# Performance work log

Hardware: AMD Instinct MI355X
Metric: run time of the kernel (lower is better)

Reference implementation:

```python
import jax, jax.numpy as jnp
import numpy as np

D, H, HD, F, A, P, NB, MD = 1024, 16, 64, 2816, 64, 30, 32, 128
B, L = 4, 1024


def _rel_bucket(rel, num_buckets=NB, max_distance=MD):
    # T5 relative position bucket, bidirectional=False (decoder self-attn)
    rel = -jnp.minimum(rel, 0)
    max_exact = num_buckets // 2
    is_small = rel < max_exact
    large = max_exact + (
        jnp.log(jnp.maximum(rel, 1).astype(jnp.float32) / max_exact)
        / np.log(max_distance / max_exact)
        * (num_buckets - max_exact)
    ).astype(jnp.int32)
    large = jnp.minimum(large, num_buckets - 1)
    return jnp.where(is_small, rel, large)


def _rmsnorm(x, scale, eps=1e-6):
    var = jnp.mean(jnp.square(x), axis=-1, keepdims=True)
    return x * jax.lax.rsqrt(var + eps) * scale


def _attn(x, kv, wq, wk, wv, wo, mask, bias, pk, pv):
    # x: [B,Lq,D], kv: [B,Lk,D], prefix pk/pv: [B,P,H,HD]
    hd = wq.shape[-1]
    q = jnp.einsum('bqd,dhe->bqhe', x, wq) * (hd ** -0.5)
    k = jnp.einsum('bkd,dhe->bkhe', kv, wk)
    v = jnp.einsum('bkd,dhe->bkhe', kv, wv)
    k = jnp.concatenate([pk, k], axis=1)  # prefix KV prepended
    v = jnp.concatenate([pv, v], axis=1)
    logits = jnp.einsum('bqhe,bkhe->bhqk', q, k).astype(jnp.float32)
    p = pk.shape[1]
    if bias is not None:
        logits = logits + jnp.pad(bias, ((0, 0), (0, 0), (0, 0), (p, 0)))
    mask = jnp.pad(mask, ((0, 0), (0, 0), (0, 0), (p, 0)), constant_values=True)
    logits = jnp.where(mask, logits, jnp.float32(-1e10))
    w = jax.nn.softmax(logits, axis=-1).astype(x.dtype)
    o = jnp.einsum('bhqk,bkhe->bqhe', w, v)
    return jnp.einsum('bqhe,hed->bqd', o, wo)


def setup_inputs() -> dict:
    key = jax.random.key(0)
    ks = jax.random.split(key, 24)
    s = D ** -0.5
    inp = {
        'inputs': jax.random.normal(ks[0], (B, L, D), jnp.float32),
        'encoded': jax.random.normal(ks[1], (B, L, D), jnp.float32),
        'adapter_wd': jax.random.normal(ks[2], (B, D, A), jnp.float32) * s,
        'adapter_wu': jax.random.normal(ks[3], (B, A, D), jnp.float32) * (A ** -0.5),
        'adapter_bd': jax.random.normal(ks[4], (B, A), jnp.float32) * 0.02,
        'adapter_bu': jax.random.normal(ks[5], (B, D), jnp.float32) * 0.02,
        'prefix_key': jax.random.normal(ks[6], (B, 2, P, H, HD), jnp.float32),
        'prefix_value': jax.random.normal(ks[7], (B, 2, P, H, HD), jnp.float32),
        'ln1': jnp.ones((D,), jnp.float32),
        'ln2': jnp.ones((D,), jnp.float32),
        'ln3': jnp.ones((D,), jnp.float32),
        'sa_wq': jax.random.normal(ks[8], (D, H, HD), jnp.float32) * s,
        'sa_wk': jax.random.normal(ks[9], (D, H, HD), jnp.float32) * s,
        'sa_wv': jax.random.normal(ks[10], (D, H, HD), jnp.float32) * s,
        'sa_wo': jax.random.normal(ks[11], (H, HD, D), jnp.float32) * s,
        'ca_wq': jax.random.normal(ks[12], (D, H, HD), jnp.float32) * s,
        'ca_wk': jax.random.normal(ks[13], (D, H, HD), jnp.float32) * s,
        'ca_wv': jax.random.normal(ks[14], (D, H, HD), jnp.float32) * s,
        'ca_wo': jax.random.normal(ks[15], (H, HD, D), jnp.float32) * s,
        'relpos': jax.random.normal(ks[16], (H, NB), jnp.float32) * 0.1,
        'mlp_wi0': jax.random.normal(ks[17], (D, F), jnp.float32) * s,
        'mlp_wi1': jax.random.normal(ks[18], (D, F), jnp.float32) * s,
        'mlp_wo': jax.random.normal(ks[19], (F, D), jnp.float32) * (F ** -0.5),
        'decoder_mask': jnp.broadcast_to(jnp.tril(jnp.ones((L, L), bool))[None, None], (B, 1, L, L)),
        'encoder_decoder_mask': jnp.ones((B, 1, L, L), bool),
    }
    return inp


def reference(inputs, encoded, adapter_wd, adapter_wu, adapter_bd, adapter_bu,
              prefix_key, prefix_value, ln1, ln2, ln3,
              sa_wq, sa_wk, sa_wv, sa_wo, ca_wq, ca_wk, ca_wv, ca_wo,
              relpos, mlp_wi0, mlp_wi1, mlp_wo,
              decoder_mask, encoder_decoder_mask):
    l = inputs.shape[1]
    pos = jnp.arange(l)
    buckets = _rel_bucket(pos[None, :] - pos[:, None])  # [L,L]
    bias = relpos[:, buckets][None]                      # [1,H,L,L]
    # self-attention with prefix + relative bias
    x = _rmsnorm(inputs, ln1)
    x = _attn(x, x, sa_wq, sa_wk, sa_wv, sa_wo, decoder_mask, bias,
              prefix_key[:, 0], prefix_value[:, 0])
    x = x + inputs
    # cross-attention with prefix
    y = _rmsnorm(x, ln2)
    y = _attn(y, encoded, ca_wq, ca_wk, ca_wv, ca_wo, encoder_decoder_mask, None,
              prefix_key[:, 1], prefix_value[:, 1])
    y = y + x
    # gated-gelu MLP + per-example adapter
    lz = _rmsnorm(y, ln3)
    z = (jax.nn.gelu(lz @ mlp_wi0) * (lz @ mlp_wi1)) @ mlp_wo
    az = jnp.einsum('bld,bda->bla', lz, adapter_wd) + adapter_bd[:, None]
    az = jax.nn.gelu(az)
    az = jnp.einsum('bla,bad->bld', az, adapter_wu) + adapter_bu[:, None]
    z = z + az
    return z + y
```

## Files before the change

### kernel.cpp

```cpp
#include <hip/hip_runtime.h>

typedef unsigned short u16;
typedef __attribute__((ext_vector_type(8))) __bf16 bf16x8;
typedef __attribute__((ext_vector_type(4))) float f32x4;

__device__ __forceinline__ float bf2f(u16 u) {
  union { unsigned int i; float f; } v; v.i = ((unsigned int)u) << 16; return v.f;
}
__device__ __forceinline__ u16 f2bf(float f) {
  unsigned int x = __float_as_uint(f);
  unsigned int r = (x + 0x7fffu + ((x >> 16) & 1u)) >> 16;
  return (u16)r;
}
__device__ __forceinline__ u16 f2bf_fast(float f) {
  return (u16)((__float_as_uint(f) + 0x8000u) >> 16);
}
__device__ __forceinline__ float gelu_f(float x) {
  float u = 0.7978845608028654f * (x + 0.044715f * x * x * x);
  float t = 1.0f - 2.0f / (__expf(2.0f * u) + 1.0f);
  return 0.5f * x * (1.0f + t);
}
__device__ __forceinline__ void gl_lds16(const u16* g, u16* l) {
  __builtin_amdgcn_global_load_lds(
      (const __attribute__((address_space(1))) unsigned int*)g,
      (__attribute__((address_space(3))) unsigned int*)l, 16, 0, 0);
}

__global__ __launch_bounds__(256) void cast_bf16_k(const float* __restrict__ in,
                                                   u16* __restrict__ out, int n4) {
  int i = blockIdx.x * 256 + threadIdx.x;
  if (i >= n4) return;
  float4 v = ((const float4*)in)[i];
  ushort4 o;
  o.x = f2bf(v.x); o.y = f2bf(v.y); o.z = f2bf(v.z); o.w = f2bf(v.w);
  ((ushort4*)out)[i] = o;
}

__global__ __launch_bounds__(256) void transpose_k(
    const float* __restrict__ in, u16* __restrict__ out, int R, int C,
    long isb, long osb) {
  __shared__ u16 tile[32][33];
  in += (size_t)blockIdx.z * isb;
  out += (size_t)blockIdx.z * osb;
  int c0 = blockIdx.x * 32, r0 = blockIdx.y * 32;
  int tx = threadIdx.x & 31, ty = threadIdx.x >> 5;
#pragma unroll
  for (int i = 0; i < 4; ++i) {
    int rr = r0 + ty + i * 8;
    if (rr < R && c0 + tx < C) tile[ty + i * 8][tx] = f2bf(in[(size_t)rr * C + c0 + tx]);
  }
  __syncthreads();
#pragma unroll
  for (int i = 0; i < 4; ++i) {
    int cc = c0 + ty + i * 8;
    if (cc < C && r0 + tx < R) out[(size_t)cc * R + r0 + tx] = tile[tx][ty + i * 8];
  }
}

__global__ __launch_bounds__(256) void bias_tab_k(const float* __restrict__ relpos,
                                                  float* __restrict__ tab) {
  int idx = blockIdx.x * 256 + threadIdx.x;
  int h = idx >> 10, d = idx & 1023;
  int bucket;
  if (d < 16) bucket = d;
  else {
    int lb = 16 + (int)(logf((float)d * (1.0f / 16.0f)) * (16.0f / logf(8.0f)));
    bucket = lb < 31 ? lb : 31;
  }
  tab[idx] = relpos[h * 32 + bucket];
}

__global__ __launch_bounds__(256) void prefix_fill_k(
    const float* __restrict__ pK, const float* __restrict__ pV,
    u16* __restrict__ Kd, u16* __restrict__ Vtd, int sSel) {
  int idx = blockIdx.x * 256 + threadIdx.x;
  int e = idx & 63, p = (idx >> 6) & 31, h = (idx >> 11) & 15, b = idx >> 15;
  int key = (p < 30) ? p : (1024 + p);
  float kv = 0.f, vv = 0.f;
  if (p < 30) {
    size_t src = ((((size_t)(b * 2 + sSel)) * 30 + p) * 16 + h) * 64 + e;
    kv = pK[src]; vv = pV[src];
  }
  Kd[(((size_t)(b * 16 + h)) * 1056 + key) * 64 + e] = f2bf(kv);
  Vtd[(((size_t)(b * 16 + h)) * 64 + e) * 1056 + key] = f2bf(vv);
}

__global__ __launch_bounds__(256) void rmsnorm_k(const float* __restrict__ in,
                                                 const float* __restrict__ scale,
                                                 u16* __restrict__ out) {
  const int D = 1024;
  size_t base = (size_t)blockIdx.x * D;
  int t = threadIdx.x;
  float x[4];
#pragma unroll
  for (int i = 0; i < 4; ++i) x[i] = in[base + t + i * 256];
  float s = x[0] * x[0] + x[1] * x[1] + x[2] * x[2] + x[3] * x[3];
#pragma unroll
  for (int off = 1; off < 64; off <<= 1) s += __shfl_xor(s, off, 64);
  __shared__ float ws4[4];
  if ((t & 63) == 0) ws4[t >> 6] = s;
  __syncthreads();
  float tot = ws4[0] + ws4[1] + ws4[2] + ws4[3];
  float r = rsqrtf(tot * (1.0f / D) + 1e-6f);
#pragma unroll
  for (int i = 0; i < 4; ++i) {
    int c = t + i * 256;
    out[base + c] = f2bf(x[i] * r * scale[c]);
  }
}

__global__ __launch_bounds__(256) void gelumul_k(const u16* __restrict__ g2,
                                                 u16* __restrict__ g) {
  int i = blockIdx.x * 256 + threadIdx.x;
  int m = i / 352, f8 = i - m * 352;
  size_t b0 = (size_t)m * 5632 + f8 * 8;
  uint4 h0 = *(const uint4*)(g2 + b0);
  uint4 h1 = *(const uint4*)(g2 + b0 + 2816);
  const u16* p0 = (const u16*)&h0;
  const u16* p1 = (const u16*)&h1;
  uint4 ov;
  u16* po = (u16*)&ov;
#pragma unroll
  for (int j = 0; j < 8; ++j) po[j] = f2bf(gelu_f(bf2f(p0[j])) * bf2f(p1[j]));
  *(uint4*)(g + (size_t)m * 2816 + f8 * 8) = ov;
}

template <int MODE>
__global__ __launch_bounds__(256) void gemm97(
    const u16* __restrict__ A, const u16* __restrict__ Bt, void* __restrict__ out,
    void* __restrict__ out2, void* __restrict__ out3,
    const float* __restrict__ res1, int M, int N, int K, float alpha) {
  const int BK = 32;
  __shared__ __align__(16) u16 As[128 * 32];
  __shared__ __align__(16) u16 Bs[128 * 32];

  const int t = threadIdx.x;
  const int wave = t >> 6, lane = t & 63;
  const int m0 = blockIdx.y * 128, n0 = blockIdx.x * 128;
  const int fr = lane & 15, fq = lane >> 4;
  const int wm = (wave >> 1) * 64, wn = (wave & 1) * 64;

  const int srow = wave * 32 + (lane >> 2);
  const int scol = (lane & 3) * 8;
  const u16* ag0 = A + (size_t)(m0 + srow) * K + scol;
  const u16* ag1 = ag0 + (size_t)16 * K;
  const u16* bg0 = Bt + (size_t)(n0 + srow) * K + scol;
  const u16* bg1 = bg0 + (size_t)16 * K;
  u16* al0 = &As[(wave * 32) * 32];
  u16* al1 = &As[(wave * 32 + 16) * 32];
  u16* bl0 = &Bs[(wave * 32) * 32];
  u16* bl1 = &Bs[(wave * 32 + 16) * 32];

  f32x4 acc[16];
#pragma unroll
  for (int i = 0; i < 16; ++i) acc[i] = (f32x4){0.f, 0.f, 0.f, 0.f};

  for (int k0 = 0; k0 < K; k0 += BK) {
    gl_lds16(ag0 + k0, al0);
    gl_lds16(ag1 + k0, al1);
    gl_lds16(bg0 + k0, bl0);
    gl_lds16(bg1 + k0, bl1);
    __syncthreads();
    bf16x8 af[4], bf[4];
#pragma unroll
    for (int i = 0; i < 4; ++i)
      af[i] = *(const bf16x8*)&As[(wm + i * 16 + fr) * 32 + fq * 8];
#pragma unroll
    for (int j = 0; j < 4; ++j)
      bf[j] = *(const bf16x8*)&Bs[(wn + j * 16 + fr) * 32 + fq * 8];
#pragma unroll
    for (int i = 0; i < 4; ++i)
#pragma unroll
      for (int j = 0; j < 4; ++j)
        acc[i * 4 + j] = __builtin_amdgcn_mfma_f32_16x16x32_bf16(
            af[i], bf[j], acc[i * 4 + j], 0, 0, 0);
    __syncthreads();
  }

#pragma unroll
  for (int i = 0; i < 4; ++i) {
#pragma unroll
    for (int rr = 0; rr < 4; ++rr) {
      long gm = (long)m0 + wm + i * 16 + fq * 4 + rr;
#pragma unroll
      for (int j = 0; j < 4; ++j) {
        int gn = n0 + wn + j * 16 + fr;
        float v = acc[i * 4 + j][rr];
        size_t oi = (size_t)gm * N + gn;
        if (MODE == 0) ((float*)out)[oi] = v;
        if (MODE == 2) ((u16*)out)[oi] = f2bf(v);
        if (MODE == 3) ((float*)out)[oi] = v + res1[oi];
        if (MODE == 8) {
          int b = (int)(gm >> 10), l = (int)(gm & 1023), h = gn >> 6, e = gn & 63;
          ((u16*)out)[(((size_t)(b * 16 + h)) * 1024 + l) * 64 + e] = f2bf(v * alpha);
        }
        if (MODE == 11) {
          int b = (int)(gm >> 10), l = (int)(gm & 1023);
          int sec = gn >> 10, nn = gn & 1023, h = nn >> 6, e = nn & 63;
          if (sec == 0)
            ((u16*)out)[(((size_t)(b * 16 + h)) * 1024 + l) * 64 + e] = f2bf(v * alpha);
          else if (sec == 1)
            ((u16*)out2)[(((size_t)(b * 16 + h)) * 1056 + 30 + l) * 64 + e] = f2bf(v);
          else
            ((u16*)out3)[(((size_t)(b * 16 + h)) * 64 + e) * 1056 + 30 + l] = f2bf(v);
        }
        if (MODE == 12) {
          int b = (int)(gm >> 10), l = (int)(gm & 1023);
          int sec = gn >> 10, nn = gn & 1023, h = nn >> 6, e = nn & 63;
          if (sec == 0)
            ((u16*)out)[(((size_t)(b * 16 + h)) * 1056 + 30 + l) * 64 + e] = f2bf(v);
          else
            ((u16*)out2)[(((size_t)(b * 16 + h)) * 64 + e) * 1056 + 30 + l] = f2bf(v);
        }
      }
    }
  }
}

template <int MODE>
__global__ __launch_bounds__(256) void gemm_bt(
    const u16* __restrict__ A, const u16* __restrict__ Bt, void* __restrict__ out,
    const float* __restrict__ res1, const float* __restrict__ res2,
    const float* __restrict__ bias, int M, int N, int K,
    long Asb, long Bsb, long bsb, long r1sb, long r2sb, long osb) {
  const int BM = 128, BK = 32, LP = 40;
  __shared__ __align__(16) u16 As[BM * LP];
  __shared__ __align__(16) u16 Bs[BM * LP];

  const int t = threadIdx.x;
  const int m0 = blockIdx.y * BM;
  const int n0 = blockIdx.x * 128;
  const int bz = blockIdx.z;
  A += (size_t)bz * Asb;
  Bt += (size_t)bz * Bsb;

  f32x4 acc[16];
#pragma unroll
  for (int i = 0; i < 16; ++i) acc[i] = (f32x4){0.f, 0.f, 0.f, 0.f};
  const int wave = t >> 6, lane = t & 63;
  const int wm = (wave >> 1) * 64, wn = (wave & 1) * 64;
  const int fr = lane & 15, fq = lane >> 4;

  for (int k0 = 0; k0 < K; k0 += BK) {
#pragma unroll
    for (int i = 0; i < 2; ++i) {
      int idx = (i * 256 + t) * 8;
      int row = idx >> 5, col = idx & 31;
      *(uint4*)&As[row * LP + col] =
          *(const uint4*)(A + (size_t)(m0 + row) * K + k0 + col);
      uint4 bv = {0u, 0u, 0u, 0u};
      if (n0 + row < N) bv = *(const uint4*)(Bt + (size_t)(n0 + row) * K + k0 + col);
      *(uint4*)&Bs[row * LP + col] = bv;
    }
    __syncthreads();
    bf16x8 af[4], bfr[4];
#pragma unroll
    for (int i = 0; i < 4; ++i)
      af[i] = *(const bf16x8*)&As[(wm + i * 16 + fr) * LP + fq * 8];
#pragma unroll
    for (int j = 0; j < 4; ++j)
      bfr[j] = *(const bf16x8*)&Bs[(wn + j * 16 + fr) * LP + fq * 8];
#pragma unroll
    for (int i = 0; i < 4; ++i)
#pragma unroll
      for (int j = 0; j < 4; ++j)
        acc[i * 4 + j] = __builtin_amdgcn_mfma_f32_16x16x32_bf16(
            af[i], bfr[j], acc[i * 4 + j], 0, 0, 0);
    __syncthreads();
  }

#pragma unroll
  for (int i = 0; i < 4; ++i) {
#pragma unroll
    for (int rr = 0; rr < 4; ++rr) {
      long gm = (long)m0 + wm + i * 16 + fq * 4 + rr;
#pragma unroll
      for (int j = 0; j < 4; ++j) {
        int gn = n0 + wn + j * 16 + fr;
        if (gn >= N) continue;
        float v = acc[i * 4 + j][rr];
        size_t oi = (size_t)bz * osb + (size_t)gm * N + gn;
        size_t ri = (size_t)gm * N + gn;
        if (MODE == 6) ((u16*)out)[oi] = f2bf(gelu_f(v + bias[(size_t)bz * bsb + gn]));
        if (MODE == 7)
          ((float*)out)[oi] = v + bias[(size_t)bz * bsb + gn] +
                              res1[(size_t)bz * r1sb + ri] +
                              res2[(size_t)bz * r2sb + ri];
      }
    }
  }
}

template <bool IS_SELF>
__global__ __launch_bounds__(256) void fattn_k(
    const u16* __restrict__ Qg, const u16* __restrict__ Kg,
    const u16* __restrict__ Vtg, const float* __restrict__ bias_tab,
    u16* __restrict__ Out) {
  const int L = 1024, P = 30, KC = 1056;
  const int flat = blockIdx.x;
  const int wg = (flat & 7) * 64 + (flat >> 3);
  const int q0b = (wg & 7) * 128;
  const int h = (wg >> 3) & 15, b = wg >> 7;
  const int t = threadIdx.x, wave = t >> 6, lane = t & 63;
  const int fr = lane & 15, fq = lane >> 4;
  const int q0w = q0b + wave * 32;

  __shared__ float bTs[IS_SELF ? 1024 : 4];
  __shared__ __align__(16) u16 Ps[4][32][40];

  if (IS_SELF) {
#pragma unroll
    for (int i = 0; i < 4; ++i) bTs[t + i * 256] = bias_tab[h * 1024 + t + i * 256];
    __syncthreads();
  }

  const u16* qptr = Qg + (((size_t)(b * 16 + h)) * L + q0w + fr) * 64 + fq * 8;
  bf16x8 qa0 = *(const bf16x8*)qptr;
  bf16x8 qa1 = *(const bf16x8*)(qptr + 32);
  bf16x8 qb0 = *(const bf16x8*)(qptr + 16 * 64);
  bf16x8 qb1 = *(const bf16x8*)(qptr + 16 * 64 + 32);

  f32x4 oA[4], oB[4];
#pragma unroll
  for (int i = 0; i < 4; ++i) {
    oA[i] = (f32x4){0.f, 0.f, 0.f, 0.f};
    oB[i] = (f32x4){0.f, 0.f, 0.f, 0.f};
  }
  f32x4 olA = (f32x4){0.f, 0.f, 0.f, 0.f};
  f32x4 olB = (f32x4){0.f, 0.f, 0.f, 0.f};
  bf16x8 ones;
  {
    u16 one = 0x3F80;
#pragma unroll
    for (int i = 0; i < 8; ++i) ((u16*)&ones)[i] = one;
  }

  const int nk = IS_SELF ? (P + q0b + 128) : (P + L);
  const int nch = (nk + 31) >> 5;
  const u16* kp = Kg + ((size_t)(b * 16 + h)) * KC * 64 + (size_t)fr * 64 + fq * 8;
  const u16* vp = Vtg + ((size_t)(b * 16 + h)) * 64 * KC + (size_t)fr * KC + fq * 8;

  bf16x8 kf0 = *(const bf16x8*)(kp + 0);
  bf16x8 kf1 = *(const bf16x8*)(kp + 32);
  bf16x8 kf2 = *(const bf16x8*)(kp + 16 * 64);
  bf16x8 kf3 = *(const bf16x8*)(kp + 16 * 64 + 32);

  auto smax = [&](f32x4* s, int k0, int qoff, int rb) {
    const bool full = IS_SELF ? (k0 >= 32 && k0 + 31 - P <= qoff)
                              : (k0 + 31 < P + L);
    if (full) {
      if (IS_SELF) {
#pragma unroll
        for (int reg = 0; reg < 4; ++reg) {
          const int qq = qoff + fq * 4 + reg;
          s[0][reg] += bTs[qq - (k0 + fr - P)];
          s[1][reg] += bTs[qq - (k0 + 16 + fr - P)];
        }
      }
    } else {
#pragma unroll
      for (int reg = 0; reg < 4; ++reg) {
        const int qq = qoff + fq * 4 + reg;
#pragma unroll
        for (int t2 = 0; t2 < 2; ++t2) {
          const int kvi = k0 + t2 * 16 + fr;
          float sv = s[t2][reg];
          if (IS_SELF) {
            const int lk = kvi - P;
            if (lk >= 0) {
              if (lk <= qq) sv += bTs[qq - lk];
              else sv = -3.0e38f;
            }
          } else {
            if (kvi >= P + L) sv = -3.0e38f;
          }
          s[t2][reg] = sv;
        }
      }
    }
#pragma unroll
    for (int reg = 0; reg < 4; ++reg) {
      Ps[wave][rb + fq * 4 + reg][fr] = f2bf_fast(__expf(s[0][reg]));
      Ps[wave][rb + fq * 4 + reg][16 + fr] = f2bf_fast(__expf(s[1][reg]));
    }
  };

  for (int ch = 0; ch < nch; ++ch) {
    const int k0 = ch * 32;
    bf16x8 vf0 = *(const bf16x8*)(vp + 0 * 16 * KC + k0);
    bf16x8 vf1 = *(const bf16x8*)(vp + 1 * 16 * KC + k0);
    bf16x8 vf2 = *(const bf16x8*)(vp + 2 * 16 * KC + k0);
    bf16x8 vf3 = *(const bf16x8*)(vp + 3 * 16 * KC + k0);
    const int k0n = (ch + 1 < nch) ? (k0 + 32) : 0;
    bf16x8 kn0 = *(const bf16x8*)(kp + (size_t)k0n * 64);
    bf16x8 kn1 = *(const bf16x8*)(kp + (size_t)k0n * 64 + 32);
    bf16x8 kn2 = *(const bf16x8*)(kp + (size_t)(k0n + 16) * 64);
    bf16x8 kn3 = *(const bf16x8*)(kp + (size_t)(k0n + 16) * 64 + 32);

    f32x4 sA[2], sB[2];
    sA[0] = (f32x4){0.f, 0.f, 0.f, 0.f};
    sA[1] = (f32x4){0.f, 0.f, 0.f, 0.f};
    sB[0] = (f32x4){0.f, 0.f, 0.f, 0.f};
    sB[1] = (f32x4){0.f, 0.f, 0.f, 0.f};
    sA[0] = __builtin_amdgcn_mfma_f32_16x16x32_bf16(qa0, kf0, sA[0], 0, 0, 0);
    sA[0] = __builtin_amdgcn_mfma_f32_16x16x32_bf16(qa1, kf1, sA[0], 0, 0, 0);
    sA[1] = __builtin_amdgcn_mfma_f32_16x16x32_bf16(qa0, kf2, sA[1], 0, 0, 0);
    sA[1] = __builtin_amdgcn_mfma_f32_16x16x32_bf16(qa1, kf3, sA[1], 0, 0, 0);
    sB[0] = __builtin_amdgcn_mfma_f32_16x16x32_bf16(qb0, kf0, sB[0], 0, 0, 0);
    sB[0] = __builtin_amdgcn_mfma_f32_16x16x32_bf16(qb1, kf1, sB[0], 0, 0, 0);
    sB[1] = __builtin_amdgcn_mfma_f32_16x16x32_bf16(qb0, kf2, sB[1], 0, 0, 0);
    sB[1] = __builtin_amdgcn_mfma_f32_16x16x32_bf16(qb1, kf3, sB[1], 0, 0, 0);

    smax(sA, k0, q0w, 0);
    smax(sB, k0, q0w + 16, 16);
    __asm__ volatile("s_waitcnt lgkmcnt(0)" ::: "memory");
    bf16x8 paA = *(const bf16x8*)&Ps[wave][fr][fq * 8];
    bf16x8 paB = *(const bf16x8*)&Ps[wave][16 + fr][fq * 8];

    oA[0] = __builtin_amdgcn_mfma_f32_16x16x32_bf16(paA, vf0, oA[0], 0, 0, 0);
    oA[1] = __builtin_amdgcn_mfma_f32_16x16x32_bf16(paA, vf1, oA[1], 0, 0, 0);
    oA[2] = __builtin_amdgcn_mfma_f32_16x16x32_bf16(paA, vf2, oA[2], 0, 0, 0);
    oA[3] = __builtin_amdgcn_mfma_f32_16x16x32_bf16(paA, vf3, oA[3], 0, 0, 0);
    olA   = __builtin_amdgcn_mfma_f32_16x16x32_bf16(paA, ones, olA, 0, 0, 0);
    oB[0] = __builtin_amdgcn_mfma_f32_16x16x32_bf16(paB, vf0, oB[0], 0, 0, 0);
    oB[1] = __builtin_amdgcn_mfma_f32_16x16x32_bf16(paB, vf1, oB[1], 0, 0, 0);
    oB[2] = __builtin_amdgcn_mfma_f32_16x16x32_bf16(paB, vf2, oB[2], 0, 0, 0);
    oB[3] = __builtin_amdgcn_mfma_f32_16x16x32_bf16(paB, vf3, oB[3], 0, 0, 0);
    olB   = __builtin_amdgcn_mfma_f32_16x16x32_bf16(paB, ones, olB, 0, 0, 0);

    kf0 = kn0; kf1 = kn1; kf2 = kn2; kf3 = kn3;
  }

  float invA[4], invB[4];
#pragma unroll
  for (int reg = 0; reg < 4; ++reg) {
    invA[reg] = 1.0f / olA[reg];
    invB[reg] = 1.0f / olB[reg];
  }
#pragma unroll
  for (int dt = 0; dt < 4; ++dt) {
#pragma unroll
    for (int reg = 0; reg < 4; ++reg) {
      size_t rowA = (size_t)(b * L + q0w + fq * 4 + reg);
      Out[(rowA * 16 + h) * 64 + dt * 16 + fr] = f2bf(oA[dt][reg] * invA[reg]);
      size_t rowB = rowA + 16;
      Out[(rowB * 16 + h) * 64 + dt * 16 + fr] = f2bf(oB[dt][reg] * invB[reg]);
    }
  }
}

extern "C" void kernel_launch(void* const* d_in, const int* in_sizes, int n_in,
                              void* d_out, int out_size, void* d_ws, size_t ws_size,
                              hipStream_t stream) {
  const int B = 4, L = 1024, D = 1024, H = 16, F = 2816, AD = 64;
  const int M = B * L;
  const int KC = 1056;

  const float* inputs  = (const float*)d_in[0];
  const float* encoded = (const float*)d_in[1];
  const float* a_wd    = (const float*)d_in[2];
  const float* a_wu    = (const float*)d_in[3];
  const float* a_bd    = (const float*)d_in[4];
  const float* a_bu    = (const float*)d_in[5];
  const float* pK      = (const float*)d_in[6];
  const float* pV      = (const float*)d_in[7];
  const float* ln1     = (const float*)d_in[8];
  const float* ln2     = (const float*)d_in[9];
  const float* ln3     = (const float*)d_in[10];
  const float* sa_wq   = (const float*)d_in[11];
  const float* sa_wk   = (const float*)d_in[12];
  const float* sa_wv   = (const float*)d_in[13];
  const float* sa_wo   = (const float*)d_in[14];
  const float* ca_wq   = (const float*)d_in[15];
  const float* ca_wk   = (const float*)d_in[16];
  const float* ca_wv   = (const float*)d_in[17];
  const float* ca_wo   = (const float*)d_in[18];
  const float* relpos  = (const float*)d_in[19];
  const float* wi0     = (const float*)d_in[20];
  const float* wi1     = (const float*)d_in[21];
  const float* wom     = (const float*)d_in[22];

  char* w = (char*)d_ws;
  size_t used = 0;
  auto alloc = [&](size_t bytes) {
    char* p = w + used;
    used += (bytes + 255) & ~(size_t)255;
    return p;
  };
  u16* wqkvT  = (u16*)alloc((size_t)3072 * 1024 * 2);
  u16* woT    = (u16*)alloc((size_t)D * 1024 * 2);
  u16* cqT    = (u16*)alloc((size_t)D * 1024 * 2);
  u16* ckvT   = (u16*)alloc((size_t)2048 * 1024 * 2);
  u16* coT    = (u16*)alloc((size_t)D * 1024 * 2);
  u16* wi01T  = (u16*)alloc((size_t)5632 * 1024 * 2);
  u16* womT   = (u16*)alloc((size_t)D * F * 2);
  u16* wdT    = (u16*)alloc((size_t)B * AD * D * 2);
  u16* wuT    = (u16*)alloc((size_t)B * D * AD * 2);
  float* bT   = (float*)alloc((size_t)H * 1024 * 4);
  u16* enc16  = (u16*)alloc((size_t)M * D * 2);
  u16* xn     = (u16*)alloc((size_t)M * D * 2);
  u16* lz     = (u16*)alloc((size_t)M * D * 2);
  u16* Kc     = (u16*)alloc((size_t)B * H * KC * 64 * 2);
  u16* Vtc    = (u16*)alloc((size_t)B * H * 64 * KC * 2);
  u16* qh     = (u16*)alloc((size_t)B * H * L * 64 * 2);
  u16* ao     = (u16*)alloc((size_t)M * D * 2);
  float* xf   = (float*)alloc((size_t)M * D * 4);
  float* yf   = (float*)alloc((size_t)M * D * 4);
  u16* az1    = (u16*)alloc((size_t)B * 1024 * AD * 2);
  u16* g2     = Kc;
  u16* g      = enc16;
  float* zf   = (float*)Kc;
  if (used > ws_size) return;

  dim3 tb(256);
  auto T = [&](const float* src, u16* dst, int R, int C, int nb, long sb) {
    transpose_k<<<dim3((C + 31) / 32, (R + 31) / 32, nb), tb, 0, stream>>>(
        src, dst, R, C, sb, sb);
  };
  T(sa_wq, wqkvT, D, 1024, 1, 0);
  T(sa_wk, wqkvT + (size_t)1024 * 1024, D, 1024, 1, 0);
  T(sa_wv, wqkvT + (size_t)2048 * 1024, D, 1024, 1, 0);
  T(sa_wo, woT, 1024, D, 1, 0);
  T(ca_wq, cqT, D, 1024, 1, 0);
  T(ca_wk, ckvT, D, 1024, 1, 0);
  T(ca_wv, ckvT + (size_t)1024 * 1024, D, 1024, 1, 0);
  T(ca_wo, coT, 1024, D, 1, 0);
  T(wi0, wi01T, D, F, 1, 0);
  T(wi1, wi01T + (size_t)2816 * 1024, D, F, 1, 0);
  T(wom, womT, F, D, 1, 0);
  T(a_wd, wdT, D, AD, B, (long)D * AD);
  T(a_wu, wuT, AD, D, B, (long)AD * D);
  bias_tab_k<<<dim3(64), tb, 0, stream>>>(relpos, bT);
  cast_bf16_k<<<dim3(M * D / 4 / 256), tb, 0, stream>>>(encoded, enc16, M * D / 4);

#define G97(MODE, Ap, Btp, Op, O2, O3, R1, Nn, Kk, al)                         \
  gemm97<MODE><<<dim3((Nn) / 128, M / 128), tb, 0, stream>>>(                  \
      (const u16*)(Ap), (const u16*)(Btp), (void*)(Op), (void*)(O2),           \
      (void*)(O3), (const float*)(R1), M, Nn, Kk, al)

  rmsnorm_k<<<dim3(M), tb, 0, stream>>>(inputs, ln1, xn);
  G97(11, xn, wqkvT, qh, Kc, Vtc, nullptr, 3072, D, 0.125f);
  prefix_fill_k<<<dim3(512), tb, 0, stream>>>(pK, pV, Kc, Vtc, 0);
  fattn_k<true><<<dim3(512), tb, 0, stream>>>(qh, Kc, Vtc, bT, ao);
  G97(3, ao, woT, xf, nullptr, nullptr, inputs, 1024, D, 1.f);
  rmsnorm_k<<<dim3(M), tb, 0, stream>>>(xf, ln2, xn);
  G97(8, xn, cqT, qh, nullptr, nullptr, nullptr, 1024, D, 0.125f);
  G97(12, enc16, ckvT, Kc, Vtc, nullptr, nullptr, 2048, D, 1.f);
  prefix_fill_k<<<dim3(512), tb, 0, stream>>>(pK, pV, Kc, Vtc, 1);
  fattn_k<false><<<dim3(512), tb, 0, stream>>>(qh, Kc, Vtc, nullptr, ao);
  G97(3, ao, coT, yf, nullptr, nullptr, xf, 1024, D, 1.f);
  rmsnorm_k<<<dim3(M), tb, 0, stream>>>(yf, ln3, lz);
  gemm_bt<6><<<dim3(1, 8, B), tb, 0, stream>>>(
      lz, wdT, az1, nullptr, nullptr, a_bd, 1024, AD, D,
      (long)1024 * D, (long)AD * D, (long)AD, 0, 0, (long)1024 * AD);
  G97(2, lz, wi01T, g2, nullptr, nullptr, nullptr, 5632, D, 1.f);
  gelumul_k<<<dim3(5632), tb, 0, stream>>>(g2, g);
  G97(0, g, womT, zf, nullptr, nullptr, nullptr, 1024, F, 1.f);
  gemm_bt<7><<<dim3(8, 8, B), tb, 0, stream>>>(
      az1, wuT, d_out, zf, yf, a_bu, 1024, 1024, AD,
      (long)1024 * AD, (long)D * AD, (long)1024, (long)1024 * 1024,
      (long)1024 * 1024, (long)1024 * 1024);
#undef G97
  (void)in_sizes; (void)n_in; (void)out_size;
}
```

Measured before the change: 754.2 us.

## Split-K the MLP down-projection and remap GEMM workgroups across XCDs

The MLP down-projection GEMM (K=2816) now runs as a two-way split-K. Each half writes its own fp32 partial buffer, and the two partials are summed in the epilogue of the final adapter GEMM, which gains a third residual input. This raises the number of workgroups for a GEMM whose grid is only about one wave on the device. Separately, every gemm97 launch now remaps its linear workgroup id in chunks of eight, so neighbouring output tiles are grouped and may share L2 better. The cost is an extra 16 MB fp32 partial written and read back, and the second partial buffer reuses workspace that overlaps buffers which must already be dead.

```diff
diff --git a/kernel.cpp b/kernel.cpp
--- a/kernel.cpp
+++ b/kernel.cpp
@@ -129,22 +129,26 @@
 __global__ __launch_bounds__(256) void gemm97(
     const u16* __restrict__ A, const u16* __restrict__ Bt, void* __restrict__ out,
     void* __restrict__ out2, void* __restrict__ out3,
-    const float* __restrict__ res1, int M, int N, int K, float alpha) {
+    const float* __restrict__ res1, int M, int N, int K, int Ks, float alpha) {
   const int BK = 32;
   __shared__ __align__(16) u16 As[128 * 32];
   __shared__ __align__(16) u16 Bs[128 * 32];
 
   const int t = threadIdx.x;
   const int wave = t >> 6, lane = t & 63;
-  const int m0 = blockIdx.y * 128, n0 = blockIdx.x * 128;
+  int wgid = blockIdx.y * gridDim.x + blockIdx.x;
+  const int cpx = (gridDim.x * gridDim.y) >> 3;
+  wgid = (wgid & 7) * cpx + (wgid >> 3);
+  const int m0 = (wgid / gridDim.x) * 128, n0 = (wgid % gridDim.x) * 128;
+  const int kbase = blockIdx.z * Ks;
   const int fr = lane & 15, fq = lane >> 4;
   const int wm = (wave >> 1) * 64, wn = (wave & 1) * 64;
 
   const int srow = wave * 32 + (lane >> 2);
   const int scol = (lane & 3) * 8;
-  const u16* ag0 = A + (size_t)(m0 + srow) * K + scol;
+  const u16* ag0 = A + (size_t)(m0 + srow) * K + kbase + scol;
   const u16* ag1 = ag0 + (size_t)16 * K;
-  const u16* bg0 = Bt + (size_t)(n0 + srow) * K + scol;
+  const u16* bg0 = Bt + (size_t)(n0 + srow) * K + kbase + scol;
   const u16* bg1 = bg0 + (size_t)16 * K;
   u16* al0 = &As[(wave * 32) * 32];
   u16* al1 = &As[(wave * 32 + 16) * 32];
@@ -155,7 +159,7 @@
 #pragma unroll
   for (int i = 0; i < 16; ++i) acc[i] = (f32x4){0.f, 0.f, 0.f, 0.f};
 
-  for (int k0 = 0; k0 < K; k0 += BK) {
+  for (int k0 = 0; k0 < Ks; k0 += BK) {
     gl_lds16(ag0 + k0, al0);
     gl_lds16(ag1 + k0, al1);
     gl_lds16(bg0 + k0, bl0);
@@ -188,6 +192,10 @@
         float v = acc[i * 4 + j][rr];
         size_t oi = (size_t)gm * N + gn;
         if (MODE == 0) ((float*)out)[oi] = v;
+        if (MODE == 1) {
+          float* po = blockIdx.z ? (float*)out2 : (float*)out;
+          po[oi] = v;
+        }
         if (MODE == 2) ((u16*)out)[oi] = f2bf(v);
         if (MODE == 3) ((float*)out)[oi] = v + res1[oi];
         if (MODE == 8) {
@@ -221,8 +229,9 @@
 __global__ __launch_bounds__(256) void gemm_bt(
     const u16* __restrict__ A, const u16* __restrict__ Bt, void* __restrict__ out,
     const float* __restrict__ res1, const float* __restrict__ res2,
-    const float* __restrict__ bias, int M, int N, int K,
-    long Asb, long Bsb, long bsb, long r1sb, long r2sb, long osb) {
+    const float* __restrict__ res3, const float* __restrict__ bias,
+    int M, int N, int K,
+    long Asb, long Bsb, long bsb, long r1sb, long r2sb, long r3sb, long osb) {
   const int BM = 128, BK = 32, LP = 40;
   __shared__ __align__(16) u16 As[BM * LP];
   __shared__ __align__(16) u16 Bs[BM * LP];
@@ -285,7 +294,8 @@
         if (MODE == 7)
           ((float*)out)[oi] = v + bias[(size_t)bz * bsb + gn] +
                               res1[(size_t)bz * r1sb + ri] +
-                              res2[(size_t)bz * r2sb + ri];
+                              res2[(size_t)bz * r2sb + ri] +
+                              res3[(size_t)bz * r3sb + ri];
       }
     }
   }
@@ -509,7 +519,8 @@
   u16* az1    = (u16*)alloc((size_t)B * 1024 * AD * 2);
   u16* g2     = Kc;
   u16* g      = enc16;
-  float* zf   = (float*)Kc;
+  float* zf0  = (float*)Kc;
+  float* zf1  = (float*)Kc + (size_t)M * D;
   if (used > ws_size) return;
 
   dim3 tb(256);
@@ -536,7 +547,7 @@
 #define G97(MODE, Ap, Btp, Op, O2, O3, R1, Nn, Kk, al)                         \
   gemm97<MODE><<<dim3((Nn) / 128, M / 128), tb, 0, stream>>>(                  \
       (const u16*)(Ap), (const u16*)(Btp), (void*)(Op), (void*)(O2),           \
-      (void*)(O3), (const float*)(R1), M, Nn, Kk, al)
+      (void*)(O3), (const float*)(R1), M, Nn, Kk, Kk, al)
 
   rmsnorm_k<<<dim3(M), tb, 0, stream>>>(inputs, ln1, xn);
   G97(11, xn, wqkvT, qh, Kc, Vtc, nullptr, 3072, D, 0.125f);
@@ -551,15 +562,17 @@
   G97(3, ao, coT, yf, nullptr, nullptr, xf, 1024, D, 1.f);
   rmsnorm_k<<<dim3(M), tb, 0, stream>>>(yf, ln3, lz);
   gemm_bt<6><<<dim3(1, 8, B), tb, 0, stream>>>(
-      lz, wdT, az1, nullptr, nullptr, a_bd, 1024, AD, D,
-      (long)1024 * D, (long)AD * D, (long)AD, 0, 0, (long)1024 * AD);
+      lz, wdT, az1, nullptr, nullptr, nullptr, a_bd, 1024, AD, D,
+      (long)1024 * D, (long)AD * D, (long)AD, 0, 0, 0, (long)1024 * AD);
   G97(2, lz, wi01T, g2, nullptr, nullptr, nullptr, 5632, D, 1.f);
   gelumul_k<<<dim3(5632), tb, 0, stream>>>(g2, g);
-  G97(0, g, womT, zf, nullptr, nullptr, nullptr, 1024, F, 1.f);
+  gemm97<1><<<dim3(8, M / 128, 2), tb, 0, stream>>>(
+      (const u16*)g, (const u16*)womT, (void*)zf0, (void*)zf1, nullptr,
+      nullptr, M, 1024, 2816, 1408, 1.f);
   gemm_bt<7><<<dim3(8, 8, B), tb, 0, stream>>>(
-      az1, wuT, d_out, zf, yf, a_bu, 1024, 1024, AD,
+      az1, wuT, d_out, zf0, zf1, yf, a_bu, 1024, 1024, AD,
       (long)1024 * AD, (long)D * AD, (long)1024, (long)1024 * 1024,
-      (long)1024 * 1024, (long)1024 * 1024);
+      (long)1024 * 1024, (long)1024 * 1024, (long)1024 * 1024);
 #undef G97
   (void)in_sizes; (void)n_in; (void)out_size;
 }
```

New measurement: 718.0 us. 4.8% less time.
